# Optimization experiments

Measured on AMD Instinct MI355X. Metric: run time of the kernel, lower is better.

Reference implementation:

```python
import jax, jax.numpy as jnp
from jax import lax
import numpy as np

I, H, B, S = 512, 1024, 64, 512


def setup_inputs() -> dict:
    key = jax.random.key(0)
    ks = jax.random.split(key, 10)
    xav = lambda k, shape: jax.random.uniform(k, shape, jnp.float32, -1.0, 1.0) * jnp.sqrt(6.0 / (shape[0] + shape[1]))
    return {
        "x": jax.random.normal(ks[0], (B, S, I), jnp.float32),
        "wii": xav(ks[1], (I, H)), "bii": jnp.zeros((H,), jnp.float32),
        "whi": xav(ks[2], (H, H)), "bhi": jnp.zeros((H,), jnp.float32),
        "wif": xav(ks[3], (I, H)), "bif": jnp.zeros((H,), jnp.float32),
        "whf": xav(ks[4], (H, H)), "bhf": jnp.zeros((H,), jnp.float32),
        "wig": xav(ks[5], (I, H)), "big": jnp.zeros((H,), jnp.float32),
        "whg": xav(ks[6], (H, H)), "bhg": jnp.zeros((H,), jnp.float32),
        "wio": xav(ks[7], (I, H)), "bio": jnp.zeros((H,), jnp.float32),
        "who": xav(ks[8], (H, H)), "bho": jnp.zeros((H,), jnp.float32),
    }


def reference(x, wii, bii, whi, bhi, wif, bif, whf, bhf,
              wig, big, whg, bhg, wio, bio, who, bho):
    b, s, _ = x.shape
    h = wii.shape[1]
    # Fuse the four per-gate GEMMs into single (I,4H) / (H,4H) GEMMs — same math.
    Wx = jnp.concatenate([wii, wif, wig, wio], axis=1)   # (I, 4H)
    Wh = jnp.concatenate([whi, whf, whg, who], axis=1)   # (H, 4H)
    bb = jnp.concatenate([bii + bhi, bif + bhf, big + bhg, bio + bho])  # (4H,)
    xs = jnp.swapaxes(x, 0, 1)                            # (S, B, I)
    x_proj = jnp.einsum('sbi,ik->sbk', xs, Wx) + bb       # (S, B, 4H)

    def step(carry, xp):
        h_t, c_t = carry
        gates = xp + h_t @ Wh                             # (B, 4H)
        i_t, f_t, g_t, o_t = jnp.split(gates, 4, axis=-1)
        i_t = jax.nn.sigmoid(i_t)
        f_t = jax.nn.sigmoid(f_t)
        g_t = jnp.tanh(g_t)
        o_t = jax.nn.sigmoid(o_t)
        c_t = f_t * c_t + i_t * g_t
        h_t = o_t * jnp.tanh(c_t)
        return (h_t, c_t), None

    h0 = jnp.zeros((b, h), x.dtype)
    c0 = jnp.zeros((b, h), x.dtype)
    (h_T, c_T), _ = lax.scan(step, (h0, c0), x_proj)
    return (h_T, c_T)
```

## Files before the change

kernel.cpp:

```cpp
#include <hip/hip_runtime.h>
#include <hip/hip_bf16.h>
#include <stdint.h>

typedef __bf16 bf16_t;
typedef bf16_t bf16x8 __attribute__((ext_vector_type(8)));
typedef float  f32x4  __attribute__((ext_vector_type(4)));
typedef float  f32x16 __attribute__((ext_vector_type(16)));

#define I_DIM 512
#define H_DIM 1024
#define B_DIM 64
#define S_DIM 512
#define G4    4096
#define CHUNK 32
#define NCHUNK (S_DIM / CHUNK)

#define O_WXT   0x0000000ULL
#define O_WHTF  0x0400000ULL
#define O_BIAS  0x0C00000ULL
#define O_CST   0x0C10000ULL
#define O_HBUF  0x0D00000ULL
#define O_BAR   0x0D40000ULL
#define O_XP    0x1200000ULL

__device__ __forceinline__ float sigm(float x)      { return 1.f / (1.f + __expf(-x)); }
__device__ __forceinline__ float tanh_fast(float x) { return 1.f - 2.f / (__expf(2.f * x) + 1.f); }


__global__ void k_pack_wx(const float* __restrict__ w0, const float* __restrict__ w1,
                          const float* __restrict__ w2, const float* __restrict__ w3,
                          bf16_t* __restrict__ wxt) {
    int tid = blockIdx.x * 256 + threadIdx.x;
    int k = tid >> 12;
    int p = tid & 4095;
    int q = p >> 5, g = (p >> 3) & 3, jj = p & 7;
    int j = q * 8 + jj;
    const float* src = (g == 0) ? w0 : (g == 1) ? w1 : (g == 2) ? w2 : w3;
    wxt[(size_t)p * I_DIM + k] = (bf16_t)src[k * H_DIM + j];
}

__global__ void k_pack_whf(const float* __restrict__ w0, const float* __restrict__ w1,
                           const float* __restrict__ w2, const float* __restrict__ w3,
                           bf16_t* __restrict__ whtf) {
    int idx = blockIdx.x * 256 + threadIdx.x;
    int e    = idx & 7;
    int lane = (idx >> 3) & 63;
    int ks   = (idx >> 9) & 63;
    int q    = idx >> 15;
    int k = ks * 16 + (lane >> 5) * 8 + e;
    int c = lane & 31;
    int g = c >> 3, jj = c & 7;
    int j = q * 8 + jj;
    const float* src = (g == 0) ? w0 : (g == 1) ? w1 : (g == 2) ? w2 : w3;
    whtf[idx] = (bf16_t)src[k * H_DIM + j];
}

__global__ void k_pack_bias(const float* bi0, const float* bh0, const float* bi1, const float* bh1,
                            const float* bi2, const float* bh2, const float* bi3, const float* bh3,
                            float* __restrict__ bias) {
    int p = blockIdx.x * 256 + threadIdx.x;
    int q = p >> 5, g = (p >> 3) & 3, jj = p & 7;
    int j = q * 8 + jj;
    const float* a = (g == 0) ? bi0 : (g == 1) ? bi1 : (g == 2) ? bi2 : bi3;
    const float* b = (g == 0) ? bh0 : (g == 1) ? bh1 : (g == 2) ? bh2 : bh3;
    bias[p] = a[j] + b[j];
}

__global__ __launch_bounds__(256, 2) void k_xproj(
    const float* __restrict__ x, const bf16_t* __restrict__ wxt,
    const float* __restrict__ bias, bf16_t* __restrict__ xp, int r_base)
{
    __shared__ __align__(16) bf16_t Al[8 * 64 * 8];
    __shared__ __align__(16) bf16_t Bl[8 * 64 * 8];
    const int tid = threadIdx.x;
    const int n0 = blockIdx.x * 128;
    const int r0 = r_base + blockIdx.y * 128;
    const int wv = tid >> 6;
    const int lane = tid & 63;
    const int mq = wv >> 1, nq = wv & 1;
    f32x4 acc[4][4] = {};

    for (int kk = 0; kk < I_DIM; kk += 32) {
        __syncthreads();
        #pragma unroll
        for (int sidx = 0; sidx < 2; ++sidx) {
            int s = tid + sidx * 256;
            int mt = s >> 6, l = s & 63;
            int m = l & 15, kb = (l >> 4) * 8;
            int r = r0 + mt * 16 + m;
            int b = r & 63, si = r >> 6;
            const float* gp = x + ((size_t)(b * S_DIM + si)) * I_DIM + kk + kb;
            float4 v0 = *(const float4*)gp;
            float4 v1 = *(const float4*)(gp + 4);
            bf16x8 a;
            a[0] = (bf16_t)v0.x; a[1] = (bf16_t)v0.y; a[2] = (bf16_t)v0.z; a[3] = (bf16_t)v0.w;
            a[4] = (bf16_t)v1.x; a[5] = (bf16_t)v1.y; a[6] = (bf16_t)v1.z; a[7] = (bf16_t)v1.w;
            *(bf16x8*)&Al[s * 8] = a;
            bf16x8 bv = *(const bf16x8*)(wxt + (size_t)(n0 + mt * 16 + m) * I_DIM + kk + kb);
            *(bf16x8*)&Bl[s * 8] = bv;
        }
        __syncthreads();
        bf16x8 af[4], bfr[4];
        #pragma unroll
        for (int mt = 0; mt < 4; ++mt) af[mt]  = *(bf16x8*)&Al[((mq * 4 + mt) * 64 + lane) * 8];
        #pragma unroll
        for (int nt = 0; nt < 4; ++nt) bfr[nt] = *(bf16x8*)&Bl[((nq * 4 + nt) * 64 + lane) * 8];
        #pragma unroll
        for (int mt = 0; mt < 4; ++mt)
            #pragma unroll
            for (int nt = 0; nt < 4; ++nt)
                acc[mt][nt] = __builtin_amdgcn_mfma_f32_16x16x32_bf16(af[mt], bfr[nt], acc[mt][nt], 0, 0, 0);
    }
    const int l15 = lane & 15, quad = lane >> 4;
    #pragma unroll
    for (int nt = 0; nt < 4; ++nt) {
        int col = n0 + nq * 64 + nt * 16 + l15;
        float bv = bias[col];
        #pragma unroll
        for (int mt = 0; mt < 4; ++mt)
            #pragma unroll
            for (int r = 0; r < 4; ++r) {
                int row = r0 - r_base + mq * 64 + mt * 16 + quad * 4 + r;
                xp[(size_t)row * G4 + col] = (bf16_t)(acc[mt][nt][r] + bv);
            }
    }
}

__global__ __launch_bounds__(256, 1) void k_steps(
    const bf16_t* __restrict__ whtf, const bf16_t* __restrict__ xp_c,
    bf16_t* __restrict__ hbuf, float* __restrict__ cstbuf,
    float* __restrict__ out, uint32_t* __restrict__ bar,
    int t_base, int ep_base, int write_out_last)
{
    __shared__ float Pl[4][16][64];
    __shared__ __align__(16) bf16_t Hlds[256];
    const int tid  = threadIdx.x;
    const int w    = tid >> 6;
    const int lane = tid & 63;
    const int bid  = blockIdx.x;
    const int q    = bid & 127;
    const int bh   = bid >> 7;

    const int col  = lane & 31;
    const int ksel = lane >> 5;
    const int gt   = (lane >> 3) & 3;
    const int jj   = lane & 7;

    int rrow[4];
    #pragma unroll
    for (int e = 0; e < 4; ++e) rrow[e] = e + 8 * w + 4 * ksel;

    const bf16_t* bb = whtf + ((size_t)q << 15) + (w << 13) + (lane << 3);
    bf16x8 bfr[16];
    #pragma unroll
    for (int i = 0; i < 16; ++i) bfr[i] = *(const bf16x8*)(bb + i * 512);

    float cst[4] = {0.f, 0.f, 0.f, 0.f};
    if (gt == 0) {
        #pragma unroll
        for (int e = 0; e < 4; ++e)
            cst[e] = cstbuf[(bh * 32 + rrow[e]) * H_DIM + q * 8 + jj];
    }

    const int abase = (bh << 15) + (w << 13) + (lane << 3);

    for (int tl = 0; tl < CHUNK; ++tl) {
        const bf16_t* xp_t = xp_c + (size_t)(tl * 64) * G4;
        uint64_t* hsrc = (uint64_t*)(hbuf + (((t_base + tl) & 1) << 16) + abase);

        uint64_t hl0[16], hl1[16];
        #pragma unroll
        for (int i = 0; i < 16; ++i) {
            hl0[i] = __hip_atomic_load(hsrc + i * 128,     __ATOMIC_RELAXED, __HIP_MEMORY_SCOPE_AGENT);
            hl1[i] = __hip_atomic_load(hsrc + i * 128 + 1, __ATOMIC_RELAXED, __HIP_MEMORY_SCOPE_AGENT);
        }

        bf16_t xpr[4];
        #pragma unroll
        for (int e = 0; e < 4; ++e)
            xpr[e] = xp_t[(size_t)(bh * 32 + rrow[e]) * G4 + q * 32 + col];

        struct U2 { uint64_t a, b; };
        f32x16 acc0 = {}, acc1 = {}, acc2 = {}, acc3 = {};
        #pragma unroll
        for (int i = 0; i < 16; i += 4) {
            U2 t0{hl0[i + 0], hl1[i + 0]};
            U2 t1{hl0[i + 1], hl1[i + 1]};
            U2 t2{hl0[i + 2], hl1[i + 2]};
            U2 t3{hl0[i + 3], hl1[i + 3]};
            acc0 = __builtin_amdgcn_mfma_f32_32x32x16_bf16(__builtin_bit_cast(bf16x8, t0), bfr[i + 0], acc0, 0, 0, 0);
            acc1 = __builtin_amdgcn_mfma_f32_32x32x16_bf16(__builtin_bit_cast(bf16x8, t1), bfr[i + 1], acc1, 0, 0, 0);
            acc2 = __builtin_amdgcn_mfma_f32_32x32x16_bf16(__builtin_bit_cast(bf16x8, t2), bfr[i + 2], acc2, 0, 0, 0);
            acc3 = __builtin_amdgcn_mfma_f32_32x32x16_bf16(__builtin_bit_cast(bf16x8, t3), bfr[i + 3], acc3, 0, 0, 0);
        }
        f32x16 accs = acc0 + acc1 + acc2 + acc3;

        #pragma unroll
        for (int e = 0; e < 16; ++e) Pl[w][e][lane] = accs[e];
        __syncthreads();

        #pragma unroll
        for (int e = 0; e < 4; ++e) {
            int eg = w * 4 + e;
            float pre = Pl[0][eg][lane] + Pl[1][eg][lane] + Pl[2][eg][lane] + Pl[3][eg][lane];
            pre += (float)xpr[e];
            float a = (gt == 2) ? tanh_fast(pre) : sigm(pre);

            float fv = __shfl_xor(a, 8, 64);
            float gv = __shfl_xor(a, 16, 64);
            float ov = __shfl_xor(a, 24, 64);
            if (gt == 0) {
                float cn = fv * cst[e] + a * gv;
                float hv = ov * tanh_fast(cn);
                cst[e] = cn;
                Hlds[rrow[e] * 8 + jj] = (bf16_t)hv;
                if (write_out_last && tl == CHUNK - 1) {
                    int rowg = bh * 32 + rrow[e];
                    int j = q * 8 + jj;
                    out[rowg * H_DIM + j] = hv;
                    out[65536 + rowg * H_DIM + j] = cn;
                }
            }
        }
        __syncthreads();

        if (w == 0) {
            uint64_t v = *(const uint64_t*)&Hlds[lane * 4];
            uint64_t* hdst = (uint64_t*)(hbuf + (((t_base + tl + 1) & 1) << 16));
            __hip_atomic_store(hdst + (bh << 13) + (q << 6) + lane, v,
                               __ATOMIC_RELAXED, __HIP_MEMORY_SCOPE_AGENT);
        }

        if (tl < CHUNK - 1) {
            __syncthreads();
            if (tid == 0) {
                uint32_t old = __hip_atomic_fetch_add(&bar[(bid & 7) * 64], 1u,
                                                      __ATOMIC_RELAXED, __HIP_MEMORY_SCOPE_AGENT);
                if ((old & 31u) == 31u) {
                    uint32_t old2 = __hip_atomic_fetch_add(&bar[512], 1u,
                                                           __ATOMIC_RELAXED, __HIP_MEMORY_SCOPE_AGENT);
                    if ((old2 & 7u) == 7u)
                        __hip_atomic_fetch_add(&bar[576], 1u,
                                               __ATOMIC_RELAXED, __HIP_MEMORY_SCOPE_AGENT);
                }
                uint32_t target = (uint32_t)(ep_base + tl + 1);
                while (__hip_atomic_load(&bar[576], __ATOMIC_RELAXED, __HIP_MEMORY_SCOPE_AGENT) < target) {}
            }
            __syncthreads();
        }
    }

    if (gt == 0) {
        #pragma unroll
        for (int e = 0; e < 4; ++e)
            cstbuf[(bh * 32 + rrow[e]) * H_DIM + q * 8 + jj] = cst[e];
    }
}

extern "C" void kernel_launch(void* const* d_in, const int* in_sizes, int n_in,
                              void* d_out, int out_size, void* d_ws, size_t ws_size,
                              hipStream_t stream) {
    const float* x   = (const float*)d_in[0];
    const float* wii = (const float*)d_in[1];
    const float* bii = (const float*)d_in[2];
    const float* whi = (const float*)d_in[3];
    const float* bhi = (const float*)d_in[4];
    const float* wif = (const float*)d_in[5];
    const float* bif = (const float*)d_in[6];
    const float* whf = (const float*)d_in[7];
    const float* bhf = (const float*)d_in[8];
    const float* wig = (const float*)d_in[9];
    const float* big = (const float*)d_in[10];
    const float* whg = (const float*)d_in[11];
    const float* bhg = (const float*)d_in[12];
    const float* wio = (const float*)d_in[13];
    const float* bio = (const float*)d_in[14];
    const float* who = (const float*)d_in[15];
    const float* bho = (const float*)d_in[16];

    char* ws = (char*)d_ws;
    bf16_t*   wxt  = (bf16_t*)(ws + O_WXT);
    bf16_t*   whtf = (bf16_t*)(ws + O_WHTF);
    float*    bias = (float*)(ws + O_BIAS);
    float*    cstb = (float*)(ws + O_CST);
    bf16_t*   hbuf = (bf16_t*)(ws + O_HBUF);
    uint32_t* bar  = (uint32_t*)(ws + O_BAR);
    bf16_t*   xp   = (bf16_t*)(ws + O_XP);

    hipMemsetAsync(hbuf, 0, 128 * 1024, stream);
    hipMemsetAsync(cstb, 0, 256 * 1024, stream);
    hipMemsetAsync(bar,  0, 4096, stream);

    k_pack_wx<<<8192, 256, 0, stream>>>(wii, wif, wig, wio, wxt);
    k_pack_whf<<<16384, 256, 0, stream>>>(whi, whf, whg, who, whtf);
    k_pack_bias<<<16, 256, 0, stream>>>(bii, bhi, bif, bhf, big, bhg, bio, bho, bias);

    float* out = (float*)d_out;
    for (int c = 0; c < NCHUNK; ++c) {
        k_xproj<<<dim3(32, CHUNK * 64 / 128), 256, 0, stream>>>(x, wxt, bias, xp, c * CHUNK * 64);
        int t_base  = c * CHUNK;
        int ep_base = c * (CHUNK - 1);
        int wol     = (c == NCHUNK - 1) ? 1 : 0;
        void* args[] = { (void*)&whtf, (void*)&xp, (void*)&hbuf, (void*)&cstb,
                         (void*)&out, (void*)&bar, (void*)&t_base, (void*)&ep_base, (void*)&wol };
        hipError_t err = hipLaunchCooperativeKernel((const void*)k_steps, dim3(256), dim3(256),
                                                    args, 0, stream);
        if (err != hipSuccess) {
            k_steps<<<256, 256, 0, stream>>>(whtf, xp, hbuf, cstb, out, bar,
                                             t_base, ep_base, wol);
        }
    }
}
```

Baseline: 3.344 ms.

## Replace grid-wide barrier with per-batch-half producer flags in LSTM step kernel

Drops the hierarchical atomic grid barrier between recurrent steps. Each block now publishes a per-block step flag after storing its slice of h, and consumers wait only on the 128 flags of their own batch half before loading h. The xp load is moved ahead of the wait so its latency overlaps the spin. Correctness now depends on relaxed atomics plus an explicit s_waitcnt to order the h store before the flag store, and the h buffer indexing and memset size change with it.

```diff
diff --git a/kernel.cpp b/kernel.cpp
--- a/kernel.cpp
+++ b/kernel.cpp
@@ -20,7 +20,7 @@
 #define O_BIAS  0x0C00000ULL
 #define O_CST   0x0C10000ULL
 #define O_HBUF  0x0D00000ULL
-#define O_BAR   0x0D40000ULL
+#define O_FLG   0x0D40000ULL
 #define O_XP    0x1200000ULL
 
 __device__ __forceinline__ float sigm(float x)      { return 1.f / (1.f + __expf(-x)); }
@@ -129,8 +129,8 @@
 __global__ __launch_bounds__(256, 1) void k_steps(
     const bf16_t* __restrict__ whtf, const bf16_t* __restrict__ xp_c,
     bf16_t* __restrict__ hbuf, float* __restrict__ cstbuf,
-    float* __restrict__ out, uint32_t* __restrict__ bar,
-    int t_base, int ep_base, int write_out_last)
+    float* __restrict__ out, uint32_t* __restrict__ flags,
+    int t_base, int write_out_last)
 {
     __shared__ float Pl[4][16][64];
     __shared__ __align__(16) bf16_t Hlds[256];
@@ -165,20 +165,33 @@
     const int abase = (bh << 15) + (w << 13) + (lane << 3);
 
     for (int tl = 0; tl < CHUNK; ++tl) {
+        const int gstep = t_base + tl;
+
         const bf16_t* xp_t = xp_c + (size_t)(tl * 64) * G4;
-        uint64_t* hsrc = (uint64_t*)(hbuf + (((t_base + tl) & 1) << 16) + abase);
-
+        bf16_t xpr[4];
+        #pragma unroll
+        for (int e = 0; e < 4; ++e)
+            xpr[e] = xp_t[(size_t)(bh * 32 + rrow[e]) * G4 + q * 32 + col];
+
+        {
+            const uint32_t target = (uint32_t)gstep;
+            for (;;) {
+                int ok = 1;
+                if (tid < 128)
+                    ok = (__hip_atomic_load(&flags[(bh << 7) + tid], __ATOMIC_RELAXED,
+                                            __HIP_MEMORY_SCOPE_AGENT) >= target);
+                if (__syncthreads_and(ok)) break;
+            }
+        }
+        asm volatile("" ::: "memory");
+
+        const uint64_t* hsrc = (const uint64_t*)(hbuf + ((gstep & 1) << 16) + abase);
         uint64_t hl0[16], hl1[16];
         #pragma unroll
         for (int i = 0; i < 16; ++i) {
             hl0[i] = __hip_atomic_load(hsrc + i * 128,     __ATOMIC_RELAXED, __HIP_MEMORY_SCOPE_AGENT);
             hl1[i] = __hip_atomic_load(hsrc + i * 128 + 1, __ATOMIC_RELAXED, __HIP_MEMORY_SCOPE_AGENT);
         }
-
-        bf16_t xpr[4];
-        #pragma unroll
-        for (int e = 0; e < 4; ++e)
-            xpr[e] = xp_t[(size_t)(bh * 32 + rrow[e]) * G4 + q * 32 + col];
 
         struct U2 { uint64_t a, b; };
         f32x16 acc0 = {}, acc1 = {}, acc2 = {}, acc3 = {};
@@ -226,27 +239,13 @@
 
         if (w == 0) {
             uint64_t v = *(const uint64_t*)&Hlds[lane * 4];
-            uint64_t* hdst = (uint64_t*)(hbuf + (((t_base + tl + 1) & 1) << 16));
-            __hip_atomic_store(hdst + (bh << 13) + (q << 6) + lane, v,
-                               __ATOMIC_RELAXED, __HIP_MEMORY_SCOPE_AGENT);
-        }
-
-        if (tl < CHUNK - 1) {
-            __syncthreads();
-            if (tid == 0) {
-                uint32_t old = __hip_atomic_fetch_add(&bar[(bid & 7) * 64], 1u,
-                                                      __ATOMIC_RELAXED, __HIP_MEMORY_SCOPE_AGENT);
-                if ((old & 31u) == 31u) {
-                    uint32_t old2 = __hip_atomic_fetch_add(&bar[512], 1u,
-                                                           __ATOMIC_RELAXED, __HIP_MEMORY_SCOPE_AGENT);
-                    if ((old2 & 7u) == 7u)
-                        __hip_atomic_fetch_add(&bar[576], 1u,
-                                               __ATOMIC_RELAXED, __HIP_MEMORY_SCOPE_AGENT);
-                }
-                uint32_t target = (uint32_t)(ep_base + tl + 1);
-                while (__hip_atomic_load(&bar[576], __ATOMIC_RELAXED, __HIP_MEMORY_SCOPE_AGENT) < target) {}
-            }
-            __syncthreads();
+            uint64_t* hdst = (uint64_t*)hbuf + (((gstep + 1) & 1) << 14)
+                           + (bh << 13) + (q << 6) + lane;
+            __hip_atomic_store(hdst, v, __ATOMIC_RELAXED, __HIP_MEMORY_SCOPE_AGENT);
+            asm volatile("s_waitcnt vmcnt(0)" ::: "memory");
+            if (lane == 0)
+                __hip_atomic_store(&flags[(bh << 7) + q], (uint32_t)(gstep + 1),
+                                   __ATOMIC_RELAXED, __HIP_MEMORY_SCOPE_AGENT);
         }
     }
 
@@ -284,12 +283,12 @@
     float*    bias = (float*)(ws + O_BIAS);
     float*    cstb = (float*)(ws + O_CST);
     bf16_t*   hbuf = (bf16_t*)(ws + O_HBUF);
-    uint32_t* bar  = (uint32_t*)(ws + O_BAR);
+    uint32_t* flg  = (uint32_t*)(ws + O_FLG);
     bf16_t*   xp   = (bf16_t*)(ws + O_XP);
 
-    hipMemsetAsync(hbuf, 0, 128 * 1024, stream);
+    hipMemsetAsync(hbuf, 0, 256 * 1024, stream);
     hipMemsetAsync(cstb, 0, 256 * 1024, stream);
-    hipMemsetAsync(bar,  0, 4096, stream);
+    hipMemsetAsync(flg,  0, 4096, stream);
 
     k_pack_wx<<<8192, 256, 0, stream>>>(wii, wif, wig, wio, wxt);
     k_pack_whf<<<16384, 256, 0, stream>>>(whi, whf, whg, who, whtf);
@@ -298,16 +297,14 @@
     float* out = (float*)d_out;
     for (int c = 0; c < NCHUNK; ++c) {
         k_xproj<<<dim3(32, CHUNK * 64 / 128), 256, 0, stream>>>(x, wxt, bias, xp, c * CHUNK * 64);
-        int t_base  = c * CHUNK;
-        int ep_base = c * (CHUNK - 1);
-        int wol     = (c == NCHUNK - 1) ? 1 : 0;
+        int t_base = c * CHUNK;
+        int wol    = (c == NCHUNK - 1) ? 1 : 0;
         void* args[] = { (void*)&whtf, (void*)&xp, (void*)&hbuf, (void*)&cstb,
-                         (void*)&out, (void*)&bar, (void*)&t_base, (void*)&ep_base, (void*)&wol };
+                         (void*)&out, (void*)&flg, (void*)&t_base, (void*)&wol };
         hipError_t err = hipLaunchCooperativeKernel((const void*)k_steps, dim3(256), dim3(256),
                                                     args, 0, stream);
         if (err != hipSuccess) {
-            k_steps<<<256, 256, 0, stream>>>(whtf, xp, hbuf, cstb, out, bar,
-                                             t_base, ep_base, wol);
-        }
-    }
-}
+            k_steps<<<256, 256, 0, stream>>>(whtf, xp, hbuf, cstb, out, flg, t_base, wol);
+        }
+    }
+}
```

Result: slower. 4.789 ms (+43.2%).

## Fuse input projection and recurrence into one persistent producer/consumer kernel

Applied to the files above, without the earlier changes.

Replaces the per-chunk pair of launches (xproj GEMM then cooperative step kernel) with a single cooperative kernel of 512 blocks. 256 blocks run the recurrence while 256 producer blocks compute the input projection into a double-buffered slot, signalling through flag counters. This lets the projection overlap the serial recurrence and removes the launch overhead and the c-state spill and reload between chunks. The grid barrier is also split per batch half, so each half synchronises only its own 128 blocks. Risks include co-residency requirements for 512 blocks, spin contention, and producer blocks taking compute units from the recurrence.

```diff
diff --git a/kernel.cpp b/kernel.cpp
--- a/kernel.cpp
+++ b/kernel.cpp
@@ -12,16 +12,19 @@
 #define B_DIM 64
 #define S_DIM 512
 #define G4    4096
-#define CHUNK 32
+#define CHUNK 16
 #define NCHUNK (S_DIM / CHUNK)
+#define XPSLOT_ELEMS ((size_t)CHUNK * 64 * G4)
 
 #define O_WXT   0x0000000ULL
 #define O_WHTF  0x0400000ULL
 #define O_BIAS  0x0C00000ULL
-#define O_CST   0x0C10000ULL
 #define O_HBUF  0x0D00000ULL
 #define O_BAR   0x0D40000ULL
 #define O_XP    0x1200000ULL
+
+#define XPD_IDX(c)  (2048 + (c) * 64)
+#define CONS_IDX(c) (4096 + (c) * 64)
 
 __device__ __forceinline__ float sigm(float x)      { return 1.f / (1.f + __expf(-x)); }
 __device__ __forceinline__ float tanh_fast(float x) { return 1.f - 2.f / (__expf(2.f * x) + 1.f); }
@@ -66,75 +69,95 @@
     bias[p] = a[j] + b[j];
 }
 
-__global__ __launch_bounds__(256, 2) void k_xproj(
+__global__ __launch_bounds__(256, 2) void k_mega(
     const float* __restrict__ x, const bf16_t* __restrict__ wxt,
-    const float* __restrict__ bias, bf16_t* __restrict__ xp, int r_base)
-{
-    __shared__ __align__(16) bf16_t Al[8 * 64 * 8];
-    __shared__ __align__(16) bf16_t Bl[8 * 64 * 8];
-    const int tid = threadIdx.x;
-    const int n0 = blockIdx.x * 128;
-    const int r0 = r_base + blockIdx.y * 128;
-    const int wv = tid >> 6;
-    const int lane = tid & 63;
-    const int mq = wv >> 1, nq = wv & 1;
-    f32x4 acc[4][4] = {};
-
-    for (int kk = 0; kk < I_DIM; kk += 32) {
-        __syncthreads();
-        #pragma unroll
-        for (int sidx = 0; sidx < 2; ++sidx) {
-            int s = tid + sidx * 256;
-            int mt = s >> 6, l = s & 63;
-            int m = l & 15, kb = (l >> 4) * 8;
-            int r = r0 + mt * 16 + m;
-            int b = r & 63, si = r >> 6;
-            const float* gp = x + ((size_t)(b * S_DIM + si)) * I_DIM + kk + kb;
-            float4 v0 = *(const float4*)gp;
-            float4 v1 = *(const float4*)(gp + 4);
-            bf16x8 a;
-            a[0] = (bf16_t)v0.x; a[1] = (bf16_t)v0.y; a[2] = (bf16_t)v0.z; a[3] = (bf16_t)v0.w;
-            a[4] = (bf16_t)v1.x; a[5] = (bf16_t)v1.y; a[6] = (bf16_t)v1.z; a[7] = (bf16_t)v1.w;
-            *(bf16x8*)&Al[s * 8] = a;
-            bf16x8 bv = *(const bf16x8*)(wxt + (size_t)(n0 + mt * 16 + m) * I_DIM + kk + kb);
-            *(bf16x8*)&Bl[s * 8] = bv;
-        }
-        __syncthreads();
-        bf16x8 af[4], bfr[4];
-        #pragma unroll
-        for (int mt = 0; mt < 4; ++mt) af[mt]  = *(bf16x8*)&Al[((mq * 4 + mt) * 64 + lane) * 8];
-        #pragma unroll
-        for (int nt = 0; nt < 4; ++nt) bfr[nt] = *(bf16x8*)&Bl[((nq * 4 + nt) * 64 + lane) * 8];
-        #pragma unroll
-        for (int mt = 0; mt < 4; ++mt)
-            #pragma unroll
-            for (int nt = 0; nt < 4; ++nt)
-                acc[mt][nt] = __builtin_amdgcn_mfma_f32_16x16x32_bf16(af[mt], bfr[nt], acc[mt][nt], 0, 0, 0);
-    }
-    const int l15 = lane & 15, quad = lane >> 4;
-    #pragma unroll
-    for (int nt = 0; nt < 4; ++nt) {
-        int col = n0 + nq * 64 + nt * 16 + l15;
-        float bv = bias[col];
-        #pragma unroll
-        for (int mt = 0; mt < 4; ++mt)
-            #pragma unroll
-            for (int r = 0; r < 4; ++r) {
-                int row = r0 - r_base + mq * 64 + mt * 16 + quad * 4 + r;
-                xp[(size_t)row * G4 + col] = (bf16_t)(acc[mt][nt][r] + bv);
-            }
-    }
-}
-
-__global__ __launch_bounds__(256, 1) void k_steps(
-    const bf16_t* __restrict__ whtf, const bf16_t* __restrict__ xp_c,
-    bf16_t* __restrict__ hbuf, float* __restrict__ cstbuf,
-    float* __restrict__ out, uint32_t* __restrict__ bar,
-    int t_base, int ep_base, int write_out_last)
+    const float* __restrict__ bias, const bf16_t* __restrict__ whtf,
+    bf16_t* __restrict__ xp, bf16_t* __restrict__ hbuf,
+    float* __restrict__ out, uint32_t* __restrict__ bar)
 {
     __shared__ float Pl[4][16][64];
     __shared__ __align__(16) bf16_t Hlds[256];
+    __shared__ __align__(16) bf16_t Al[8 * 64 * 8];
+    __shared__ __align__(16) bf16_t Bl[8 * 64 * 8];
     const int tid  = threadIdx.x;
+
+    if (blockIdx.x >= 256) {
+        const int xbid = blockIdx.x - 256;
+        const int n0 = (xbid & 31) * 128;
+        const int rt = (xbid >> 5) * 128;
+        const int wv = tid >> 6;
+        const int lane = tid & 63;
+        const int mq = wv >> 1, nq = wv & 1;
+        const int l15 = lane & 15, quad = lane >> 4;
+
+        for (int sc = 0; sc < NCHUNK; ++sc) {
+            if (sc >= 2) {
+                if (tid == 0) {
+                    while (__hip_atomic_load(&bar[CONS_IDX(sc - 2)], __ATOMIC_RELAXED,
+                                             __HIP_MEMORY_SCOPE_AGENT) < 256u)
+                        __builtin_amdgcn_s_sleep(2);
+                }
+                __syncthreads();
+            }
+            bf16_t* xps = xp + (size_t)(sc & 1) * XPSLOT_ELEMS;
+            const int r_base = sc * (CHUNK * 64);
+
+            f32x4 acc[4][4] = {};
+            for (int kk = 0; kk < I_DIM; kk += 32) {
+                __syncthreads();
+                #pragma unroll
+                for (int sidx = 0; sidx < 2; ++sidx) {
+                    int s = tid + sidx * 256;
+                    int mt = s >> 6, l = s & 63;
+                    int m = l & 15, kb = (l >> 4) * 8;
+                    int r = r_base + rt + mt * 16 + m;
+                    int b = r & 63, si = r >> 6;
+                    const float* gp = x + ((size_t)(b * S_DIM + si)) * I_DIM + kk + kb;
+                    float4 v0 = *(const float4*)gp;
+                    float4 v1 = *(const float4*)(gp + 4);
+                    bf16x8 a;
+                    a[0] = (bf16_t)v0.x; a[1] = (bf16_t)v0.y; a[2] = (bf16_t)v0.z; a[3] = (bf16_t)v0.w;
+                    a[4] = (bf16_t)v1.x; a[5] = (bf16_t)v1.y; a[6] = (bf16_t)v1.z; a[7] = (bf16_t)v1.w;
+                    *(bf16x8*)&Al[s * 8] = a;
+                    bf16x8 bv = *(const bf16x8*)(wxt + (size_t)(n0 + mt * 16 + m) * I_DIM + kk + kb);
+                    *(bf16x8*)&Bl[s * 8] = bv;
+                }
+                __syncthreads();
+                bf16x8 af[4], bfr[4];
+                #pragma unroll
+                for (int mt = 0; mt < 4; ++mt) af[mt]  = *(bf16x8*)&Al[((mq * 4 + mt) * 64 + lane) * 8];
+                #pragma unroll
+                for (int nt = 0; nt < 4; ++nt) bfr[nt] = *(bf16x8*)&Bl[((nq * 4 + nt) * 64 + lane) * 8];
+                #pragma unroll
+                for (int mt = 0; mt < 4; ++mt)
+                    #pragma unroll
+                    for (int nt = 0; nt < 4; ++nt)
+                        acc[mt][nt] = __builtin_amdgcn_mfma_f32_16x16x32_bf16(af[mt], bfr[nt], acc[mt][nt], 0, 0, 0);
+            }
+            #pragma unroll
+            for (int nt = 0; nt < 4; ++nt) {
+                int colg = n0 + nq * 64 + nt * 16 + l15;
+                float bv = bias[colg];
+                #pragma unroll
+                for (int mt = 0; mt < 4; ++mt)
+                    #pragma unroll
+                    for (int r = 0; r < 4; ++r) {
+                        int row = rt + mq * 64 + mt * 16 + quad * 4 + r;
+                        bf16_t hb = (bf16_t)(acc[mt][nt][r] + bv);
+                        __hip_atomic_store((uint16_t*)(xps + (size_t)row * G4 + colg),
+                                           __builtin_bit_cast(unsigned short, hb),
+                                           __ATOMIC_RELAXED, __HIP_MEMORY_SCOPE_AGENT);
+                    }
+            }
+            asm volatile("s_waitcnt vmcnt(0)" ::: "memory");
+            __syncthreads();
+            if (tid == 0)
+                __hip_atomic_fetch_add(&bar[XPD_IDX(sc)], 1u,
+                                       __ATOMIC_RELAXED, __HIP_MEMORY_SCOPE_AGENT);
+        }
+        return;
+    }
+
     const int w    = tid >> 6;
     const int lane = tid & 63;
     const int bid  = blockIdx.x;
@@ -146,6 +169,10 @@
     const int gt   = (lane >> 3) & 3;
     const int jj   = lane & 7;
 
+    uint32_t* grp   = bar + ((bh * 8 + (q & 7)) << 6);
+    uint32_t* root  = bar + 1024 + (bh << 6);
+    uint32_t* epoch = bar + 1152 + (bh << 6);
+
     int rrow[4];
     #pragma unroll
     for (int e = 0; e < 4; ++e) rrow[e] = e + 8 * w + 4 * ksel;
@@ -156,104 +183,111 @@
     for (int i = 0; i < 16; ++i) bfr[i] = *(const bf16x8*)(bb + i * 512);
 
     float cst[4] = {0.f, 0.f, 0.f, 0.f};
-    if (gt == 0) {
-        #pragma unroll
-        for (int e = 0; e < 4; ++e)
-            cst[e] = cstbuf[(bh * 32 + rrow[e]) * H_DIM + q * 8 + jj];
-    }
 
     const int abase = (bh << 15) + (w << 13) + (lane << 3);
 
-    for (int tl = 0; tl < CHUNK; ++tl) {
-        const bf16_t* xp_t = xp_c + (size_t)(tl * 64) * G4;
-        uint64_t* hsrc = (uint64_t*)(hbuf + (((t_base + tl) & 1) << 16) + abase);
-
-        uint64_t hl0[16], hl1[16];
-        #pragma unroll
-        for (int i = 0; i < 16; ++i) {
-            hl0[i] = __hip_atomic_load(hsrc + i * 128,     __ATOMIC_RELAXED, __HIP_MEMORY_SCOPE_AGENT);
-            hl1[i] = __hip_atomic_load(hsrc + i * 128 + 1, __ATOMIC_RELAXED, __HIP_MEMORY_SCOPE_AGENT);
-        }
-
-        bf16_t xpr[4];
-        #pragma unroll
-        for (int e = 0; e < 4; ++e)
-            xpr[e] = xp_t[(size_t)(bh * 32 + rrow[e]) * G4 + q * 32 + col];
-
-        struct U2 { uint64_t a, b; };
-        f32x16 acc0 = {}, acc1 = {}, acc2 = {}, acc3 = {};
-        #pragma unroll
-        for (int i = 0; i < 16; i += 4) {
-            U2 t0{hl0[i + 0], hl1[i + 0]};
-            U2 t1{hl0[i + 1], hl1[i + 1]};
-            U2 t2{hl0[i + 2], hl1[i + 2]};
-            U2 t3{hl0[i + 3], hl1[i + 3]};
-            acc0 = __builtin_amdgcn_mfma_f32_32x32x16_bf16(__builtin_bit_cast(bf16x8, t0), bfr[i + 0], acc0, 0, 0, 0);
-            acc1 = __builtin_amdgcn_mfma_f32_32x32x16_bf16(__builtin_bit_cast(bf16x8, t1), bfr[i + 1], acc1, 0, 0, 0);
-            acc2 = __builtin_amdgcn_mfma_f32_32x32x16_bf16(__builtin_bit_cast(bf16x8, t2), bfr[i + 2], acc2, 0, 0, 0);
-            acc3 = __builtin_amdgcn_mfma_f32_32x32x16_bf16(__builtin_bit_cast(bf16x8, t3), bfr[i + 3], acc3, 0, 0, 0);
-        }
-        f32x16 accs = acc0 + acc1 + acc2 + acc3;
-
-        #pragma unroll
-        for (int e = 0; e < 16; ++e) Pl[w][e][lane] = accs[e];
-        __syncthreads();
-
-        #pragma unroll
-        for (int e = 0; e < 4; ++e) {
-            int eg = w * 4 + e;
-            float pre = Pl[0][eg][lane] + Pl[1][eg][lane] + Pl[2][eg][lane] + Pl[3][eg][lane];
-            pre += (float)xpr[e];
-            float a = (gt == 2) ? tanh_fast(pre) : sigm(pre);
-
-            float fv = __shfl_xor(a, 8, 64);
-            float gv = __shfl_xor(a, 16, 64);
-            float ov = __shfl_xor(a, 24, 64);
-            if (gt == 0) {
-                float cn = fv * cst[e] + a * gv;
-                float hv = ov * tanh_fast(cn);
-                cst[e] = cn;
-                Hlds[rrow[e] * 8 + jj] = (bf16_t)hv;
-                if (write_out_last && tl == CHUNK - 1) {
-                    int rowg = bh * 32 + rrow[e];
-                    int j = q * 8 + jj;
-                    out[rowg * H_DIM + j] = hv;
-                    out[65536 + rowg * H_DIM + j] = cn;
-                }
-            }
+    for (int c = 0; c < NCHUNK; ++c) {
+        if (tid == 0) {
+            while (__hip_atomic_load(&bar[XPD_IDX(c)], __ATOMIC_RELAXED,
+                                     __HIP_MEMORY_SCOPE_AGENT) < 256u)
+                __builtin_amdgcn_s_sleep(2);
         }
         __syncthreads();
-
-        if (w == 0) {
-            uint64_t v = *(const uint64_t*)&Hlds[lane * 4];
-            uint64_t* hdst = (uint64_t*)(hbuf + (((t_base + tl + 1) & 1) << 16));
-            __hip_atomic_store(hdst + (bh << 13) + (q << 6) + lane, v,
-                               __ATOMIC_RELAXED, __HIP_MEMORY_SCOPE_AGENT);
+        const uint16_t* xpc = (const uint16_t*)(xp + (size_t)(c & 1) * XPSLOT_ELEMS);
+
+        for (int tl = 0; tl < CHUNK; ++tl) {
+            const int t = c * CHUNK + tl;
+
+            const uint64_t* hsrc = (const uint64_t*)(hbuf + ((t & 1) << 16) + abase);
+            uint64_t hl0[16], hl1[16];
+            #pragma unroll
+            for (int i = 0; i < 16; ++i) {
+                hl0[i] = __hip_atomic_load(hsrc + i * 128,     __ATOMIC_RELAXED, __HIP_MEMORY_SCOPE_AGENT);
+                hl1[i] = __hip_atomic_load(hsrc + i * 128 + 1, __ATOMIC_RELAXED, __HIP_MEMORY_SCOPE_AGENT);
+            }
+
+            bf16_t xpr[4];
+            #pragma unroll
+            for (int e = 0; e < 4; ++e) {
+                unsigned short v = __hip_atomic_load(
+                    &xpc[(size_t)(tl * 64 + bh * 32 + rrow[e]) * G4 + q * 32 + col],
+                    __ATOMIC_RELAXED, __HIP_MEMORY_SCOPE_AGENT);
+                xpr[e] = __builtin_bit_cast(bf16_t, v);
+            }
+
+            struct U2 { uint64_t a, b; };
+            f32x16 acc0 = {}, acc1 = {}, acc2 = {}, acc3 = {};
+            #pragma unroll
+            for (int i = 0; i < 16; i += 4) {
+                U2 t0{hl0[i + 0], hl1[i + 0]};
+                U2 t1{hl0[i + 1], hl1[i + 1]};
+                U2 t2{hl0[i + 2], hl1[i + 2]};
+                U2 t3{hl0[i + 3], hl1[i + 3]};
+                acc0 = __builtin_amdgcn_mfma_f32_32x32x16_bf16(__builtin_bit_cast(bf16x8, t0), bfr[i + 0], acc0, 0, 0, 0);
+                acc1 = __builtin_amdgcn_mfma_f32_32x32x16_bf16(__builtin_bit_cast(bf16x8, t1), bfr[i + 1], acc1, 0, 0, 0);
+                acc2 = __builtin_amdgcn_mfma_f32_32x32x16_bf16(__builtin_bit_cast(bf16x8, t2), bfr[i + 2], acc2, 0, 0, 0);
+                acc3 = __builtin_amdgcn_mfma_f32_32x32x16_bf16(__builtin_bit_cast(bf16x8, t3), bfr[i + 3], acc3, 0, 0, 0);
+            }
+            f32x16 accs = acc0 + acc1 + acc2 + acc3;
+
+            #pragma unroll
+            for (int e = 0; e < 16; ++e) Pl[w][e][lane] = accs[e];
+            __syncthreads();
+
+            #pragma unroll
+            for (int e = 0; e < 4; ++e) {
+                int eg = w * 4 + e;
+                float pre = Pl[0][eg][lane] + Pl[1][eg][lane] + Pl[2][eg][lane] + Pl[3][eg][lane];
+                pre += (float)xpr[e];
+                float a = (gt == 2) ? tanh_fast(pre) : sigm(pre);
+
+                float fv = __shfl_xor(a, 8, 64);
+                float gv = __shfl_xor(a, 16, 64);
+                float ov = __shfl_xor(a, 24, 64);
+                if (gt == 0) {
+                    float cn = fv * cst[e] + a * gv;
+                    float hv = ov * tanh_fast(cn);
+                    cst[e] = cn;
+                    Hlds[rrow[e] * 8 + jj] = (bf16_t)hv;
+                    if (t == S_DIM - 1) {
+                        int rowg = bh * 32 + rrow[e];
+                        int j = q * 8 + jj;
+                        out[rowg * H_DIM + j] = hv;
+                        out[65536 + rowg * H_DIM + j] = cn;
+                    }
+                }
+            }
+            __syncthreads();
+
+            if (w == 0) {
+                uint64_t v = *(const uint64_t*)&Hlds[lane * 4];
+                uint64_t* hdst = (uint64_t*)hbuf + (((t + 1) & 1) << 14)
+                               + (bh << 13) + (q << 6) + lane;
+                __hip_atomic_store(hdst, v, __ATOMIC_RELAXED, __HIP_MEMORY_SCOPE_AGENT);
+                if (t < S_DIM - 1) {
+                    asm volatile("s_waitcnt vmcnt(0)" ::: "memory");
+                    if (lane == 0) {
+                        uint32_t old = __hip_atomic_fetch_add(grp, 1u,
+                                                              __ATOMIC_RELAXED, __HIP_MEMORY_SCOPE_AGENT);
+                        if ((old & 15u) == 15u) {
+                            uint32_t old2 = __hip_atomic_fetch_add(root, 1u,
+                                                                   __ATOMIC_RELAXED, __HIP_MEMORY_SCOPE_AGENT);
+                            if ((old2 & 7u) == 7u)
+                                __hip_atomic_fetch_add(epoch, 1u,
+                                                       __ATOMIC_RELAXED, __HIP_MEMORY_SCOPE_AGENT);
+                        }
+                        uint32_t target = (uint32_t)(t + 1);
+                        while (__hip_atomic_load(epoch, __ATOMIC_RELAXED,
+                                                 __HIP_MEMORY_SCOPE_AGENT) < target) {}
+                    }
+                }
+            }
+            if (t < S_DIM - 1) __syncthreads();
         }
 
-        if (tl < CHUNK - 1) {
-            __syncthreads();
-            if (tid == 0) {
-                uint32_t old = __hip_atomic_fetch_add(&bar[(bid & 7) * 64], 1u,
-                                                      __ATOMIC_RELAXED, __HIP_MEMORY_SCOPE_AGENT);
-                if ((old & 31u) == 31u) {
-                    uint32_t old2 = __hip_atomic_fetch_add(&bar[512], 1u,
-                                                           __ATOMIC_RELAXED, __HIP_MEMORY_SCOPE_AGENT);
-                    if ((old2 & 7u) == 7u)
-                        __hip_atomic_fetch_add(&bar[576], 1u,
-                                               __ATOMIC_RELAXED, __HIP_MEMORY_SCOPE_AGENT);
-                }
-                uint32_t target = (uint32_t)(ep_base + tl + 1);
-                while (__hip_atomic_load(&bar[576], __ATOMIC_RELAXED, __HIP_MEMORY_SCOPE_AGENT) < target) {}
-            }
-            __syncthreads();
-        }
-    }
-
-    if (gt == 0) {
-        #pragma unroll
-        for (int e = 0; e < 4; ++e)
-            cstbuf[(bh * 32 + rrow[e]) * H_DIM + q * 8 + jj] = cst[e];
+        if (tid == 0)
+            __hip_atomic_fetch_add(&bar[CONS_IDX(c)], 1u,
+                                   __ATOMIC_RELAXED, __HIP_MEMORY_SCOPE_AGENT);
     }
 }
 
@@ -282,32 +316,23 @@
     bf16_t*   wxt  = (bf16_t*)(ws + O_WXT);
     bf16_t*   whtf = (bf16_t*)(ws + O_WHTF);
     float*    bias = (float*)(ws + O_BIAS);
-    float*    cstb = (float*)(ws + O_CST);
     bf16_t*   hbuf = (bf16_t*)(ws + O_HBUF);
     uint32_t* bar  = (uint32_t*)(ws + O_BAR);
     bf16_t*   xp   = (bf16_t*)(ws + O_XP);
 
-    hipMemsetAsync(hbuf, 0, 128 * 1024, stream);
-    hipMemsetAsync(cstb, 0, 256 * 1024, stream);
-    hipMemsetAsync(bar,  0, 4096, stream);
+    hipMemsetAsync(hbuf, 0, 256 * 1024, stream);
+    hipMemsetAsync(bar,  0, 32 * 1024, stream);
 
     k_pack_wx<<<8192, 256, 0, stream>>>(wii, wif, wig, wio, wxt);
     k_pack_whf<<<16384, 256, 0, stream>>>(whi, whf, whg, who, whtf);
     k_pack_bias<<<16, 256, 0, stream>>>(bii, bhi, bif, bhf, big, bhg, bio, bho, bias);
 
     float* out = (float*)d_out;
-    for (int c = 0; c < NCHUNK; ++c) {
-        k_xproj<<<dim3(32, CHUNK * 64 / 128), 256, 0, stream>>>(x, wxt, bias, xp, c * CHUNK * 64);
-        int t_base  = c * CHUNK;
-        int ep_base = c * (CHUNK - 1);
-        int wol     = (c == NCHUNK - 1) ? 1 : 0;
-        void* args[] = { (void*)&whtf, (void*)&xp, (void*)&hbuf, (void*)&cstb,
-                         (void*)&out, (void*)&bar, (void*)&t_base, (void*)&ep_base, (void*)&wol };
-        hipError_t err = hipLaunchCooperativeKernel((const void*)k_steps, dim3(256), dim3(256),
-                                                    args, 0, stream);
-        if (err != hipSuccess) {
-            k_steps<<<256, 256, 0, stream>>>(whtf, xp, hbuf, cstb, out, bar,
-                                             t_base, ep_base, wol);
-        }
+    void* args[] = { (void*)&x, (void*)&wxt, (void*)&bias, (void*)&whtf,
+                     (void*)&xp, (void*)&hbuf, (void*)&out, (void*)&bar };
+    hipError_t err = hipLaunchCooperativeKernel((const void*)k_mega, dim3(512), dim3(256),
+                                                args, 0, stream);
+    if (err != hipSuccess) {
+        k_mega<<<512, 256, 0, stream>>>(x, wxt, bias, whtf, xp, hbuf, out, bar);
     }
 }
```

Result: faster. 3.171 ms (-5.2%).
